# Optimization experiments

Measured on AMD Instinct MI355X. Metric: run time of the kernel, lower is better.

Reference implementation:

```python
import jax, jax.numpy as jnp
import numpy as np

B, Lq, D = 2, 4096, 768
NH, NP, NL = 6, 4, 1
Hs, Ws = 128, 128
Lf = Hs * Ws
DH = D // NH
EPS = 1e-6


def _ln(x, g, b):
    m = jnp.mean(x, -1, keepdims=True)
    v = jnp.mean(jnp.square(x - m), -1, keepdims=True)
    return (x - m) * jax.lax.rsqrt(v + EPS) * g + b


def setup_inputs() -> dict:
    key = jax.random.key(0)
    ks = jax.random.split(key, 20)
    s = 0.02
    rn = lambda k, shape, sc=s: (jax.random.normal(k, shape, jnp.float32) * sc)
    return {
        'query': jax.random.normal(ks[0], (B, Lq, D), jnp.float32),
        'reference_points': jax.random.uniform(ks[1], (B, Lq, NL, 2), jnp.float32),
        'feat': jax.random.normal(ks[2], (B, Lf, D), jnp.float32),
        'feat_other_modalities': jax.random.normal(ks[3], (B, Lq, D), jnp.float32),
        'spatial_shapes': jnp.array([[Hs, Ws]], jnp.int32),
        'level_start_index': jnp.array([0], jnp.int32),
        'qn_g': jnp.ones(D), 'qn_b': jnp.zeros(D),
        'fn_g': jnp.ones(D), 'fn_b': jnp.zeros(D),
        'W_off': rn(ks[4], (D, NH * NL * NP * 2)), 'b_off': jnp.zeros(NH * NL * NP * 2),
        'W_attn': rn(ks[5], (D, NH * NL * NP)), 'b_attn': jnp.zeros(NH * NL * NP),
        'W_val': rn(ks[6], (D, D)), 'b_val': jnp.zeros(D),
        'W_out': rn(ks[7], (D, D)), 'b_out': jnp.zeros(D),
        'gamma': rn(ks[8], (D,), 0.1),
        'qnm_g': jnp.ones(D), 'qnm_b': jnp.zeros(D),
        'fnm_g': jnp.ones(D), 'fnm_b': jnp.zeros(D),
        'ada_w0': rn(ks[9], (D, D // 4)), 'ada_b0': jnp.zeros(D // 4),
        'ada_w1': rn(ks[10], (D, D // 4)), 'ada_b1': jnp.zeros(D // 4),
        'ada_w2': rn(ks[11], (D // 4, D)), 'ada_b2': jnp.zeros(D),
        'gamma_om': rn(ks[12], (D,), 0.1),
    }


def _msdeform_attn(query_n, reference_points, feat_n, Hi, Wi,
                   W_off, b_off, W_attn, b_attn, W_val, b_val, W_out, b_out):
    Bv = query_n.shape[0]
    value = (feat_n @ W_val + b_val).reshape(Bv, Lf, NH, DH)
    value = value.transpose(0, 2, 1, 3)  # (B, NH, Lf, DH)

    off = (query_n @ W_off + b_off).reshape(Bv, Lq, NH, NL, NP, 2)
    aw = (query_n @ W_attn + b_attn).reshape(Bv, Lq, NH, NL * NP)
    aw = jax.nn.softmax(aw, axis=-1).reshape(Bv, Lq, NH, NL, NP)

    normalizer = jnp.array([Wi, Hi], jnp.float32)  # [W, H]
    loc = reference_points[:, :, None, :, None, :] + off / normalizer  # (B,Lq,NH,NL,NP,2)
    loc = loc[:, :, :, 0]  # single level -> (B, Lq, NH, NP, 2)

    # grid_sample align_corners=False, padding zeros
    x = loc[..., 0] * Wi - 0.5
    y = loc[..., 1] * Hi - 0.5
    x0 = jnp.floor(x); y0 = jnp.floor(y)
    wx1 = x - x0; wx0 = 1.0 - wx1
    wy1 = y - y0; wy0 = 1.0 - wy1
    x0i = x0.astype(jnp.int32); y0i = y0.astype(jnp.int32)
    x1i = x0i + 1; y1i = y0i + 1

    def t(a):  # (B,Lq,NH,NP) -> (B,NH,Lq,NP,1)
        return a.transpose(0, 2, 1, 3)[..., None]

    def gather(yy, xx):
        valid = (xx >= 0) & (xx < Wi) & (yy >= 0) & (yy < Hi)
        idx = jnp.clip(yy, 0, Hi - 1) * Wi + jnp.clip(xx, 0, Wi - 1)  # (B,Lq,NH,NP)
        idx = idx.transpose(0, 2, 1, 3).reshape(Bv, NH, Lq * NP)
        g = jnp.take_along_axis(value, idx[..., None], axis=2)  # (B,NH,Lq*NP,DH)
        g = g.reshape(Bv, NH, Lq, NP, DH)
        return g * t(valid.astype(jnp.float32))

    sampled = (gather(y0i, x0i) * t(wy0 * wx0) + gather(y0i, x1i) * t(wy0 * wx1)
               + gather(y1i, x0i) * t(wy1 * wx0) + gather(y1i, x1i) * t(wy1 * wx1))
    awT = aw[:, :, :, 0].transpose(0, 2, 1, 3)[..., None]  # (B,NH,Lq,NP,1)
    out = jnp.sum(sampled * awT, axis=3)  # (B,NH,Lq,DH)
    out = out.transpose(0, 2, 1, 3).reshape(Bv, Lq, D)
    return out @ W_out + b_out


def reference(query, reference_points, feat, feat_other_modalities, spatial_shapes,
              level_start_index, qn_g, qn_b, fn_g, fn_b, W_off, b_off, W_attn, b_attn,
              W_val, b_val, W_out, b_out, gamma, qnm_g, qnm_b, fnm_g, fnm_b,
              ada_w0, ada_b0, ada_w1, ada_b1, ada_w2, ada_b2, gamma_om):
    Hi = int(np.asarray(spatial_shapes)[0, 0]); Wi = int(np.asarray(spatial_shapes)[0, 1])
    query_n = _ln(query, qn_g, qn_b)
    feat_n = _ln(feat, fn_g, fn_b)
    attn = _msdeform_attn(query_n, reference_points, feat_n, Hi, Wi,
                          W_off, b_off, W_attn, b_attn, W_val, b_val, W_out, b_out)
    q = query + gamma * attn
    fom_n = _ln(feat_other_modalities, fnm_g, fnm_b)
    qn2 = _ln(q, qnm_g, qnm_b)
    p = qn2 @ ada_w0 + ada_b0
    xm = fom_n @ ada_w1 + ada_b1
    prompted = (p + xm) @ ada_w2 + ada_b2
    q = q + gamma_om * prompted
    return (q, prompted)
```

## Files before the change

kernel.cpp:

```cpp
#include <hip/hip_runtime.h>
#include <hip/hip_bf16.h>

typedef long long i64;

#define B_   2
#define LQ   4096
#define D_   768
#define NH_  6
#define NP_  4
#define DH_  128
#define LF   16384
#define NQ_ROWS (B_*LQ)
#define NF_ROWS (B_*LF)
#define QSIZE (NQ_ROWS*D_)

typedef __bf16 bf16x8 __attribute__((ext_vector_type(8)));
typedef float  f32x4  __attribute__((ext_vector_type(4)));

__device__ __forceinline__ int probe_bf(const void* probe) {
  return (*(const unsigned*)probe == 0x3F803F80u) ? 1 : 0;
}
__device__ __forceinline__ float load_in(const void* p, i64 i, int bf) {
  if (bf) return __bfloat162float(((const __hip_bfloat16*)p)[i]);
  return ((const float*)p)[i];
}
__device__ __forceinline__ float us2f(unsigned short u) {
  unsigned v = (unsigned)u << 16;
  return __uint_as_float(v);
}
__device__ __forceinline__ unsigned short f2us(float f) {
  __hip_bfloat16 h = __float2bfloat16(f);
  return *(unsigned short*)&h;
}

#define NCVT 17
struct CvtArgs { const void* src[NCVT]; const void* src2[NCVT]; float* dst[NCVT]; int n[NCVT]; const void* probe; };
__global__ void k_cvt(CvtArgs a) {
  int bf = probe_bf(a.probe);
  int ai = blockIdx.y;
  int n = a.n[ai];
  const void* s = a.src[ai];
  const void* s2 = a.src2[ai];
  float* d = a.dst[ai];
  for (int i = blockIdx.x * blockDim.x + threadIdx.x; i < n; i += gridDim.x * blockDim.x) {
    float v = load_in(s, i, bf);
    if (s2) v += load_in(s2, i, bf);
    d[i] = v;
  }
}

#define NTT 7
struct TtArgs {
  const void* src[NTT]; __hip_bfloat16* dst[NTT];
  int K[NTT]; int N[NTT]; int Nt[NTT]; int ds[NTT];
  int tileBase[NTT]; int tilesN[NTT];
  const void* probe;
};
__global__ void k_transpose(TtArgs a) {
  __shared__ float lds[64][65];
  int bf = probe_bf(a.probe);
  int t = blockIdx.x;
  int e = 0;
  #pragma unroll
  for (int i = 1; i < NTT; ++i) if (t >= a.tileBase[i]) e = i;
  int lt = t - a.tileBase[e];
  int tn = lt % a.tilesN[e], tk = lt / a.tilesN[e];
  int K = a.K[e], N = a.N[e], Nt = a.Nt[e], ds = a.ds[e];
  int k0 = tk * 64, n0 = tn * 64;
  int tid = threadIdx.x;
  int cl = tid & 63, rw = tid >> 6;
  const void* s = a.src[e];
  #pragma unroll
  for (int i = 0; i < 16; ++i) {
    int kl = rw * 16 + i;
    int n = n0 + cl;
    float v = (n < N) ? load_in(s, (i64)(k0 + kl) * N + n, bf) : 0.f;
    lds[kl][cl] = v;
  }
  __syncthreads();
  __hip_bfloat16* d = a.dst[e];
  #pragma unroll
  for (int i = 0; i < 16; ++i) {
    int nl = rw * 16 + i;
    int n = n0 + nl;
    if (n < Nt) d[(i64)n * ds + k0 + cl] = __float2bfloat16(lds[cl][nl]);
  }
}


__device__ __forceinline__ void ln_load_bf16(const void* src, i64 so, int sl, uint4* u) {
  const unsigned short* s = (const unsigned short*)src + so;
  #pragma unroll
  for (int j = 0; j < 3; ++j) u[j] = *(const uint4*)(s + (i64)(j * 32 + sl) * 8);
}
__device__ __forceinline__ void ln_load_f32(const void* src, i64 so, int sl, float4* w) {
  const float* s = (const float*)src + so;
  #pragma unroll
  for (int j = 0; j < 3; ++j) {
    w[2*j]   = *(const float4*)(s + (i64)(j * 32 + sl) * 8);
    w[2*j+1] = *(const float4*)(s + (i64)(j * 32 + sl) * 8 + 4);
  }
}
__device__ __forceinline__ void ln_unpack_bf16(const uint4* u, float* v) {
  #pragma unroll
  for (int j = 0; j < 3; ++j) {
    uint4 t = u[j];
    v[j*8+0] = us2f((unsigned short)t.x); v[j*8+1] = us2f((unsigned short)(t.x >> 16));
    v[j*8+2] = us2f((unsigned short)t.y); v[j*8+3] = us2f((unsigned short)(t.y >> 16));
    v[j*8+4] = us2f((unsigned short)t.z); v[j*8+5] = us2f((unsigned short)(t.z >> 16));
    v[j*8+6] = us2f((unsigned short)t.w); v[j*8+7] = us2f((unsigned short)(t.w >> 16));
  }
}
__device__ __forceinline__ void ln_unpack_f32(const float4* w, float* v) {
  #pragma unroll
  for (int j = 0; j < 6; ++j) {
    v[j*4+0] = w[j].x; v[j*4+1] = w[j].y; v[j*4+2] = w[j].z; v[j*4+3] = w[j].w;
  }
}
__device__ __forceinline__ void ln_finish(const float* v, const float* g, const float* b,
                                          unsigned short* dp, int sl) {
  float s1 = 0.f, s2 = 0.f;
  #pragma unroll
  for (int i = 0; i < 24; ++i) { s1 += v[i]; s2 += v[i] * v[i]; }
  #pragma unroll
  for (int o = 16; o > 0; o >>= 1) { s1 += __shfl_xor(s1, o, 64); s2 += __shfl_xor(s2, o, 64); }
  float mean = s1 * (1.f / 768.f);
  float var  = s2 * (1.f / 768.f) - mean * mean;
  float rstd = rsqrtf(var + 1e-6f);
  #pragma unroll
  for (int j = 0; j < 3; ++j) {
    int gi = (j * 32 + sl) * 8;
    float4 g0 = *(const float4*)(g + gi), g1 = *(const float4*)(g + gi + 4);
    float4 b0 = *(const float4*)(b + gi), b1 = *(const float4*)(b + gi + 4);
    uint4 o;
    o.x = (unsigned)f2us((v[j*8+0]-mean)*rstd*g0.x+b0.x) | ((unsigned)f2us((v[j*8+1]-mean)*rstd*g0.y+b0.y) << 16);
    o.y = (unsigned)f2us((v[j*8+2]-mean)*rstd*g0.z+b0.z) | ((unsigned)f2us((v[j*8+3]-mean)*rstd*g0.w+b0.w) << 16);
    o.z = (unsigned)f2us((v[j*8+4]-mean)*rstd*g1.x+b1.x) | ((unsigned)f2us((v[j*8+5]-mean)*rstd*g1.y+b1.y) << 16);
    o.w = (unsigned)f2us((v[j*8+6]-mean)*rstd*g1.z+b1.z) | ((unsigned)f2us((v[j*8+7]-mean)*rstd*g1.w+b1.w) << 16);
    *(uint4*)(dp + gi) = o;
  }
}

struct Ln3Args {
  const void* src0; const void* src1; const void* src2;
  const float *g0, *b0, *g1, *b1, *g2, *b2;
  __hip_bfloat16 *d0, *d1, *d2;
  const void* probe;
};
__device__ __forceinline__ void resolve3(const Ln3Args& a, int row,
    const void*& s, i64& so, const float*& g, const float*& b, unsigned short*& dp) {
  if (row < NF_ROWS) {
    s = a.src0; so = (i64)row * 768; g = a.g0; b = a.b0;
    dp = (unsigned short*)a.d0 + (i64)row * 768;
  } else if (row < NF_ROWS + NQ_ROWS) {
    int r = row - NF_ROWS;
    s = a.src1; so = (i64)r * 768; g = a.g1; b = a.b1;
    dp = (unsigned short*)a.d1 + (i64)r * 768;
  } else {
    int r = row - NF_ROWS - NQ_ROWS;
    s = a.src2; so = (i64)r * 768; g = a.g2; b = a.b2;
    dp = (unsigned short*)a.d2 + (i64)r * 1536 + 768;
  }
}
__global__ void k_ln3(Ln3Args a) {
  int bf = probe_bf(a.probe);
  int hw = blockIdx.x * 8 + (threadIdx.x >> 5);
  int sl = threadIdx.x & 31;
  int row = hw * 2;
  const void* s0; i64 so0; const float *g0, *b0; unsigned short* dp0;
  const void* s1; i64 so1; const float *g1, *b1; unsigned short* dp1;
  resolve3(a, row,     s0, so0, g0, b0, dp0);
  resolve3(a, row + 1, s1, so1, g1, b1, dp1);
  float v[24];
  if (bf) {
    uint4 u0[3], u1[3];
    ln_load_bf16(s0, so0, sl, u0);
    ln_load_bf16(s1, so1, sl, u1);
    ln_unpack_bf16(u0, v);
    ln_finish(v, g0, b0, dp0, sl);
    ln_unpack_bf16(u1, v);
    ln_finish(v, g1, b1, dp1, sl);
  } else {
    float4 w0[6], w1[6];
    ln_load_f32(s0, so0, sl, w0);
    ln_load_f32(s1, so1, sl, w1);
    ln_unpack_f32(w0, v);
    ln_finish(v, g0, b0, dp0, sl);
    ln_unpack_f32(w1, v);
    ln_finish(v, g1, b1, dp1, sl);
  }
}
__global__ void k_ln_q(const float* src, const float* g, const float* b, __hip_bfloat16* dst) {
  int hw = blockIdx.x * 8 + (threadIdx.x >> 5);
  int sl = threadIdx.x & 31;
  int r = hw * 2;
  float4 w0[6], w1[6];
  ln_load_f32(src, (i64)r * 768, sl, w0);
  ln_load_f32(src, (i64)(r + 1) * 768, sl, w1);
  float v[24];
  ln_unpack_f32(w0, v);
  ln_finish(v, g, b, (unsigned short*)dst + (i64)r * 1536, sl);
  ln_unpack_f32(w1, v);
  ln_finish(v, g, b, (unsigned short*)dst + (i64)(r + 1) * 1536, sl);
}

__device__ __forceinline__ void load_lds16(const void* g, void* l) {
  __builtin_amdgcn_global_load_lds((__attribute__((address_space(1))) void*)g,
                                   (__attribute__((address_space(3))) void*)l, 16, 0, 0);
}

template<int EPI>
__global__ void k_mgemm(const __hip_bfloat16* __restrict__ A, const __hip_bfloat16* __restrict__ Wt,
                        const float* __restrict__ bias, void* __restrict__ Cp,
                        int M, int N, int K, int Nx,
                        const void* aux0, const float* __restrict__ aux1, const void* probe) {
  __shared__ __align__(16) __hip_bfloat16 sm[2 * 8192];
  __hip_bfloat16* As = sm;
  __hip_bfloat16* Bs = sm + 8192;
  const int tid  = threadIdx.x;
  const int w    = tid >> 6, lane = tid & 63;
  const int quad = lane >> 4, l15 = lane & 15;
  const int f = blockIdx.x;
  const int xcd = f & 7, s8 = f >> 3;
  const int bn = (s8 % Nx) * 128;
  const int bm = (xcd + (s8 / Nx) * 8) * 128;
  const int wm = (w >> 1) * 64, wn = (w & 1) * 64;
  const int bfv = (EPI == 2 || EPI == 3) ? probe_bf(probe) : 0;

  int rowS[4], colS[4];
  #pragma unroll
  for (int j = 0; j < 4; ++j) {
    int p = j * 256 + tid;
    int r = p >> 3, pc = p & 7;
    rowS[j] = r; colS[j] = (pc ^ (r & 7)) * 8;
  }

  f32x4 acc[4][4];
  #pragma unroll
  for (int i = 0; i < 4; ++i)
    #pragma unroll
    for (int j = 0; j < 4; ++j) acc[i][j] = (f32x4){0.f, 0.f, 0.f, 0.f};

  const __hip_bfloat16* Ab = A  + (i64)bm * K;
  const __hip_bfloat16* Bb = Wt + (i64)bn * K;

  for (int k0 = 0; k0 < K; k0 += 64) {
    #pragma unroll
    for (int j = 0; j < 4; ++j) {
      load_lds16(Ab + (i64)rowS[j] * K + k0 + colS[j], As + (j * 256 + w * 64) * 8);
      load_lds16(Bb + (i64)rowS[j] * K + k0 + colS[j], Bs + (j * 256 + w * 64) * 8);
    }
    __syncthreads();
    bf16x8 af[2][4], bg[2][4];
    #pragma unroll
    for (int s = 0; s < 2; ++s) {
      #pragma unroll
      for (int i = 0; i < 4; ++i) {
        int ra = wm + i * 16 + l15;
        af[s][i] = *(const bf16x8*)(As + (ra * 8 + ((s * 4 + quad) ^ (ra & 7))) * 8);
        int rb = wn + i * 16 + l15;
        bg[s][i] = *(const bf16x8*)(Bs + (rb * 8 + ((s * 4 + quad) ^ (rb & 7))) * 8);
      }
    }
    #pragma unroll
    for (int s = 0; s < 2; ++s)
      #pragma unroll
      for (int i = 0; i < 4; ++i)
        #pragma unroll
        for (int j = 0; j < 4; ++j)
          acc[i][j] = __builtin_amdgcn_mfma_f32_16x16x32_bf16(af[s][i], bg[s][j], acc[i][j], 0, 0, 0);
    __syncthreads();
  }

  #pragma unroll
  for (int j = 0; j < 4; ++j) {
    int col = bn + wn + j * 16 + l15;
    if (col >= N) continue;
    float bv = bias[col];
    #pragma unroll
    for (int i = 0; i < 4; ++i) {
      #pragma unroll
      for (int r = 0; r < 4; ++r) {
        int row = bm + wm + i * 16 + quad * 4 + r;
        float v = acc[i][j][r] + bv;
        i64 idx = (i64)row * N + col;
        if (EPI == 0) {
          ((__hip_bfloat16*)Cp)[idx] = __float2bfloat16(v);
        } else if (EPI == 1) {
          ((float*)Cp)[idx] = v;
        } else if (EPI == 2) {
          ((float*)Cp)[idx] = load_in(aux0, idx, bfv) + aux1[col] * v;
        } else {
          float qv = ((const float*)aux0)[idx] + aux1[col] * v;
          if (bfv) {
            ((__hip_bfloat16*)Cp)[idx]         = __float2bfloat16(qv);
            ((__hip_bfloat16*)Cp)[QSIZE + idx] = __float2bfloat16(v);
          } else {
            ((float*)Cp)[idx]         = qv;
            ((float*)Cp)[QSIZE + idx] = v;
          }
        }
      }
    }
  }
}

__global__ void k_sample(const __hip_bfloat16* __restrict__ val, const float* __restrict__ ref,
                         const float* __restrict__ oa, const int* __restrict__ ss,
                         __hip_bfloat16* __restrict__ out) {
  int gw = blockIdx.x * 4 + (threadIdx.x >> 6);
  if (gw >= NQ_ROWS) return;
  int lane = threadIdx.x & 63;
  int sg = lane >> 4, sl = lane & 15;
  int bq = gw, b = bq >> 12;
  int Hi = ss[0], Wi = ss[1];
  float Wf = (float)Wi, Hf = (float)Hi;
  float rx = ref[(i64)bq*2], ry = ref[(i64)bq*2 + 1];
  const float* orow = oa + (i64)bq * 72;
  const __hip_bfloat16* vb = val + (i64)b * LF * D_;
  int cx = sg & 1, cy = sg >> 1;
  #pragma unroll
  for (int h = 0; h < NH_; ++h) {
    const float* ap = orow + 48 + h*4;
    float a0 = ap[0], a1 = ap[1], a2 = ap[2], a3 = ap[3];
    float mx = fmaxf(fmaxf(a0, a1), fmaxf(a2, a3));
    float e0 = __expf(a0-mx), e1 = __expf(a1-mx), e2 = __expf(a2-mx), e3 = __expf(a3-mx);
    float inv = 1.0f / (e0+e1+e2+e3);
    float wts[4] = {e0*inv, e1*inv, e2*inv, e3*inv};
    const float* op = orow + h*8;
    float acc[8];
    #pragma unroll
    for (int e = 0; e < 8; ++e) acc[e] = 0.f;
    #pragma unroll
    for (int p = 0; p < NP_; ++p) {
      float x = rx*Wf + op[p*2+0] - 0.5f;
      float y = ry*Hf + op[p*2+1] - 0.5f;
      float xf = floorf(x), yf = floorf(y);
      int x0 = (int)xf, y0 = (int)yf;
      float wx1 = x - xf, wy1 = y - yf;
      int xi = x0 + cx, yi = y0 + cy;
      float wgt = wts[p] * (cx ? wx1 : 1.f - wx1) * (cy ? wy1 : 1.f - wy1);
      if (xi >= 0 && xi < Wi && yi >= 0 && yi < Hi) {
        bf16x8 g = *(const bf16x8*)(vb + (i64)(yi*Wi + xi)*D_ + h*DH_ + sl*8);
        #pragma unroll
        for (int e = 0; e < 8; ++e) acc[e] += wgt * (float)g[e];
      }
    }
    #pragma unroll
    for (int e = 0; e < 8; ++e) {
      acc[e] += __shfl_xor(acc[e], 16, 64);
      acc[e] += __shfl_xor(acc[e], 32, 64);
    }
    if (sg == 0) {
      uint4 o;
      o.x = (unsigned)f2us(acc[0]) | ((unsigned)f2us(acc[1]) << 16);
      o.y = (unsigned)f2us(acc[2]) | ((unsigned)f2us(acc[3]) << 16);
      o.z = (unsigned)f2us(acc[4]) | ((unsigned)f2us(acc[5]) << 16);
      o.w = (unsigned)f2us(acc[6]) | ((unsigned)f2us(acc[7]) << 16);
      *(uint4*)(out + (i64)bq*D_ + h*DH_ + sl*8) = o;
    }
  }
}

extern "C" void kernel_launch(void* const* d_in, const int* in_sizes, int n_in,
                              void* d_out, int out_size, void* d_ws, size_t ws_size,
                              hipStream_t stream) {
  char* base = (char*)d_ws;
  size_t o = 0;
  auto alloc = [&](size_t bytes) { size_t r = o; o += (bytes + 63) & ~(size_t)63; return r; };
  auto F = [&](size_t off) { return (float*)(base + off); };
  auto H = [&](size_t off) { return (__hip_bfloat16*)(base + off); };
  const void* probe = d_in[6];

  size_t REF   = alloc(NQ_ROWS*2*4);
  size_t QN_G  = alloc(768*4); size_t QN_B = alloc(768*4);
  size_t FN_G  = alloc(768*4); size_t FN_B = alloc(768*4);
  size_t BOA   = alloc(128*4);
  size_t BVAL  = alloc(768*4); size_t BOUT = alloc(768*4);
  size_t GAMMA = alloc(768*4);
  size_t QNM_G = alloc(768*4); size_t QNM_B = alloc(768*4);
  size_t FNM_G = alloc(768*4); size_t FNM_B = alloc(768*4);
  size_t AB01  = alloc(192*4);
  size_t AB2   = alloc(768*4); size_t GOM  = alloc(768*4);
  size_t WT_VAL = alloc((size_t)768*768*2);
  size_t WT_OUT = alloc((size_t)768*768*2);
  size_t WT_OA  = alloc((size_t)128*768*2);
  size_t WT_A01 = alloc((size_t)256*1536*2);
  size_t WT_A2  = alloc((size_t)768*192*2);
  size_t FEATN  = alloc((size_t)NF_ROWS*768*2);
  size_t VALUE  = alloc((size_t)NF_ROWS*768*2);
  size_t QN     = alloc((size_t)NQ_ROWS*768*2);
  size_t QNF    = alloc((size_t)NQ_ROWS*1536*2);
  size_t ATTNP  = alloc((size_t)NQ_ROWS*768*2);
  size_t PXM    = alloc((size_t)NQ_ROWS*192*2);
  size_t OA     = alloc((size_t)NQ_ROWS*72*4);
  size_t QBUF   = alloc((size_t)QSIZE*4);

  {
    CvtArgs ca;
    const int   idx[NCVT]  = {1,6,7,8,9,11,13,15,17,18,19,20,21,22,24,28,29};
    const size_t dof[NCVT] = {REF,QN_G,QN_B,FN_G,FN_B,BOA,BOA+48*4,BVAL,BOUT,GAMMA,
                              QNM_G,QNM_B,FNM_G,FNM_B,AB01,AB2,GOM};
    for (int i = 0; i < NCVT; ++i) {
      ca.src[i] = d_in[idx[i]]; ca.src2[i] = nullptr;
      ca.dst[i] = F(dof[i]); ca.n[i] = in_sizes[idx[i]];
    }
    ca.src2[14] = d_in[26];
    ca.probe = probe;
    k_cvt<<<dim3(8, NCVT), 256, 0, stream>>>(ca);
  }
  {
    TtArgs ta;
    const int   src[NTT]  = {14, 16, 10, 12, 23, 25, 27};
    const size_t dst[NTT] = {WT_VAL, WT_OUT, WT_OA, WT_OA + (size_t)48*768*2,
                             WT_A01, WT_A01 + (size_t)768*2, WT_A2};
    const int Kk[NTT] = {768, 768, 768, 768, 768,  768, 192};
    const int Nn[NTT] = {768, 768,  48,  24, 192,  192, 768};
    const int Nt[NTT] = {768, 768,  48,  80, 256,  256, 768};
    const int Ds[NTT] = {768, 768, 768, 768, 1536, 1536, 192};
    int tb = 0;
    for (int i = 0; i < NTT; ++i) {
      ta.src[i] = d_in[src[i]]; ta.dst[i] = H(dst[i]);
      ta.K[i] = Kk[i]; ta.N[i] = Nn[i]; ta.Nt[i] = Nt[i]; ta.ds[i] = Ds[i];
      ta.tilesN[i] = (Nt[i] + 63) / 64;
      ta.tileBase[i] = tb;
      tb += ta.tilesN[i] * (Kk[i] / 64);
    }
    ta.probe = probe;
    k_transpose<<<tb, 256, 0, stream>>>(ta);
  }

  {
    Ln3Args la;
    la.src0 = d_in[2]; la.g0 = F(FN_G);  la.b0 = F(FN_B);  la.d0 = H(FEATN);
    la.src1 = d_in[0]; la.g1 = F(QN_G);  la.b1 = F(QN_B);  la.d1 = H(QN);
    la.src2 = d_in[3]; la.g2 = F(FNM_G); la.b2 = F(FNM_B); la.d2 = H(QNF);
    la.probe = probe;
    k_ln3<<<(NF_ROWS + 2*NQ_ROWS) / 16, 256, 0, stream>>>(la);
  }

  k_mgemm<0><<<256*6, 256, 0, stream>>>(H(FEATN), H(WT_VAL), F(BVAL), H(VALUE),
                                        NF_ROWS, 768, 768, 6, nullptr, nullptr, probe);
  k_mgemm<1><<<64*1, 256, 0, stream>>>(H(QN), H(WT_OA), F(BOA), F(OA),
                                       NQ_ROWS, 72, 768, 1, nullptr, nullptr, probe);
  k_sample<<<NQ_ROWS/4, 256, 0, stream>>>(H(VALUE), F(REF), F(OA), (const int*)d_in[4], H(ATTNP));
  k_mgemm<2><<<64*6, 256, 0, stream>>>(H(ATTNP), H(WT_OUT), F(BOUT), F(QBUF),
                                       NQ_ROWS, 768, 768, 6, d_in[0], F(GAMMA), probe);
  k_ln_q<<<NQ_ROWS/16, 256, 0, stream>>>(F(QBUF), F(QNM_G), F(QNM_B), H(QNF));
  k_mgemm<0><<<64*2, 256, 0, stream>>>(H(QNF), H(WT_A01), F(AB01), H(PXM),
                                       NQ_ROWS, 192, 1536, 2, nullptr, nullptr, probe);
  k_mgemm<3><<<64*6, 256, 0, stream>>>(H(PXM), H(WT_A2), F(AB2), d_out,
                                       NQ_ROWS, 768, 192, 6, F(QBUF), F(GOM), probe);
}
```

Measured before the change: 480.7 us.

## Fold layernorm of feat and query into GEMM epilogues via row stats

Instead of writing normalized bf16 feat/query, the pre-pass computes per-row rstd and -mean*rstd, and folds gamma into the transposed weights. The GEMM epilogue reconstructs LN(x)@W as rstd*acc + rc*colsum(gW) + colsum(bW) + bias. A small colsum kernel computes these vectors. With bf16 inputs the raw input is fed straight to the GEMM, skipping the normalized write. With fp32 inputs it still writes an unnormalized bf16 copy. The pre-pass is also made grid-stride with software prefetch. The trade-off is some precision loss, since unnormalized values are rounded to bf16 before the matmul.

```diff
diff --git a/kernel.cpp b/kernel.cpp
--- a/kernel.cpp
+++ b/kernel.cpp
@@ -13,6 +13,7 @@
 #define NQ_ROWS (B_*LQ)
 #define NF_ROWS (B_*LF)
 #define QSIZE (NQ_ROWS*D_)
+#define R_TOT (NF_ROWS + 2*NQ_ROWS)
 
 typedef __bf16 bf16x8 __attribute__((ext_vector_type(8)));
 typedef float  f32x4  __attribute__((ext_vector_type(4)));
@@ -52,6 +53,7 @@
 #define NTT 7
 struct TtArgs {
   const void* src[NTT]; __hip_bfloat16* dst[NTT];
+  const void* scale[NTT];
   int K[NTT]; int N[NTT]; int Nt[NTT]; int ds[NTT];
   int tileBase[NTT]; int tilesN[NTT];
   const void* probe;
@@ -70,11 +72,13 @@
   int tid = threadIdx.x;
   int cl = tid & 63, rw = tid >> 6;
   const void* s = a.src[e];
+  const void* sc = a.scale[e];
   #pragma unroll
   for (int i = 0; i < 16; ++i) {
     int kl = rw * 16 + i;
     int n = n0 + cl;
     float v = (n < N) ? load_in(s, (i64)(k0 + kl) * N + n, bf) : 0.f;
+    if (sc) v *= load_in(sc, k0 + kl, bf);
     lds[kl][cl] = v;
   }
   __syncthreads();
@@ -87,6 +91,30 @@
   }
 }
 
+#define NCS 3
+struct CsArgs {
+  const void* w[NCS]; const void* g[NCS]; const void* b[NCS];
+  float* c[NCS]; float* d[NCS];
+  int K[NCS]; int N[NCS]; int blkBase[NCS];
+  const void* probe;
+};
+__global__ void k_colsum(CsArgs a) {
+  int bf = probe_bf(a.probe);
+  int e = 0;
+  #pragma unroll
+  for (int i = 1; i < NCS; ++i) if ((int)blockIdx.x >= a.blkBase[i]) e = i;
+  int j = (blockIdx.x - a.blkBase[e]) * 256 + threadIdx.x;
+  int K = a.K[e], N = a.N[e];
+  if (j >= N) return;
+  const void* w = a.w[e]; const void* g = a.g[e]; const void* b = a.b[e];
+  float cs = 0.f, ds = 0.f;
+  for (int k = 0; k < K; ++k) {
+    float wv = load_in(w, (i64)k * N + j, bf);
+    cs += load_in(g, k, bf) * wv;
+    ds += load_in(b, k, bf) * wv;
+  }
+  a.c[e][j] = cs; a.d[e][j] = ds;
+}
 
 __device__ __forceinline__ void ln_load_bf16(const void* src, i64 so, int sl, uint4* u) {
   const unsigned short* s = (const unsigned short*)src + so;
@@ -117,8 +145,7 @@
     v[j*4+0] = w[j].x; v[j*4+1] = w[j].y; v[j*4+2] = w[j].z; v[j*4+3] = w[j].w;
   }
 }
-__device__ __forceinline__ void ln_finish(const float* v, const float* g, const float* b,
-                                          unsigned short* dp, int sl) {
+__device__ __forceinline__ void pre_stats(const float* v, float& rstd, float& rc) {
   float s1 = 0.f, s2 = 0.f;
   #pragma unroll
   for (int i = 0; i < 24; ++i) { s1 += v[i]; s2 += v[i] * v[i]; }
@@ -126,7 +153,14 @@
   for (int o = 16; o > 0; o >>= 1) { s1 += __shfl_xor(s1, o, 64); s2 += __shfl_xor(s2, o, 64); }
   float mean = s1 * (1.f / 768.f);
   float var  = s2 * (1.f / 768.f) - mean * mean;
-  float rstd = rsqrtf(var + 1e-6f);
+  rstd = rsqrtf(var + 1e-6f);
+  rc = -rstd * mean;
+}
+__device__ __forceinline__ void ln_finish(const float* v, const float* g, const float* b,
+                                          unsigned short* dp, int sl) {
+  float rstd, rc;
+  pre_stats(v, rstd, rc);
+  float mean = -rc / rstd;
   #pragma unroll
   for (int j = 0; j < 3; ++j) {
     int gi = (j * 32 + sl) * 8;
@@ -140,56 +174,83 @@
     *(uint4*)(dp + gi) = o;
   }
 }
-
-struct Ln3Args {
-  const void* src0; const void* src1; const void* src2;
-  const float *g0, *b0, *g1, *b1, *g2, *b2;
-  __hip_bfloat16 *d0, *d1, *d2;
+__device__ __forceinline__ void pack_store(const float* v, unsigned short* dp, int sl) {
+  #pragma unroll
+  for (int j = 0; j < 3; ++j) {
+    int gi = (j * 32 + sl) * 8;
+    uint4 o;
+    o.x = (unsigned)f2us(v[j*8+0]) | ((unsigned)f2us(v[j*8+1]) << 16);
+    o.y = (unsigned)f2us(v[j*8+2]) | ((unsigned)f2us(v[j*8+3]) << 16);
+    o.z = (unsigned)f2us(v[j*8+4]) | ((unsigned)f2us(v[j*8+5]) << 16);
+    o.w = (unsigned)f2us(v[j*8+6]) | ((unsigned)f2us(v[j*8+7]) << 16);
+    *(uint4*)(dp + gi) = o;
+  }
+}
+
+struct PreArgs {
+  const void* feat; const void* query; const void* fom;
+  const float *fg, *fb;
+  float* fstat; float* qstat;
+  __hip_bfloat16* feat_bf; __hip_bfloat16* q_bf;
+  __hip_bfloat16* qnf;
   const void* probe;
 };
-__device__ __forceinline__ void resolve3(const Ln3Args& a, int row,
-    const void*& s, i64& so, const float*& g, const float*& b, unsigned short*& dp) {
-  if (row < NF_ROWS) {
-    s = a.src0; so = (i64)row * 768; g = a.g0; b = a.b0;
-    dp = (unsigned short*)a.d0 + (i64)row * 768;
-  } else if (row < NF_ROWS + NQ_ROWS) {
-    int r = row - NF_ROWS;
-    s = a.src1; so = (i64)r * 768; g = a.g1; b = a.b1;
-    dp = (unsigned short*)a.d1 + (i64)r * 768;
+__device__ __forceinline__ void pre_src(const PreArgs& a, int row,
+    const void*& s, i64& so, int& kind, int& lr) {
+  if (row < NF_ROWS)                { s = a.feat;  lr = row;                       so = (i64)lr * 768; kind = 0; }
+  else if (row < NF_ROWS + NQ_ROWS) { s = a.query; lr = row - NF_ROWS;            so = (i64)lr * 768; kind = 1; }
+  else                              { s = a.fom;   lr = row - NF_ROWS - NQ_ROWS;  so = (i64)lr * 768; kind = 2; }
+}
+__global__ void k_pre(PreArgs a) {
+  int bf = probe_bf(a.probe);
+  int sl = threadIdx.x & 31;
+  int stride = gridDim.x * 8;
+  int r = blockIdx.x * 8 + (threadIdx.x >> 5);
+  if (bf) {
+    uint4 u[3]; const void* s; i64 so; int kind = 0, lr = 0;
+    if (r < R_TOT) { pre_src(a, r, s, so, kind, lr); ln_load_bf16(s, so, sl, u); }
+    while (r < R_TOT) {
+      int rn = r + stride;
+      uint4 un[3]; const void* sn; i64 son; int kn = 0, lrn = 0;
+      if (rn < R_TOT) { pre_src(a, rn, sn, son, kn, lrn); ln_load_bf16(sn, son, sl, un); }
+      float v[24];
+      ln_unpack_bf16(u, v);
+      if (kind == 2) {
+        ln_finish(v, a.fg, a.fb, (unsigned short*)a.qnf + (i64)lr * 1536 + 768, sl);
+      } else {
+        float rstd, rc; pre_stats(v, rstd, rc);
+        float* st = (kind == 0) ? a.fstat : a.qstat;
+        if (sl == 0) { st[2*lr] = rstd; st[2*lr+1] = rc; }
+      }
+      r = rn; kind = kn; lr = lrn;
+      u[0] = un[0]; u[1] = un[1]; u[2] = un[2];
+    }
   } else {
-    int r = row - NF_ROWS - NQ_ROWS;
-    s = a.src2; so = (i64)r * 768; g = a.g2; b = a.b2;
-    dp = (unsigned short*)a.d2 + (i64)r * 1536 + 768;
-  }
-}
-__global__ void k_ln3(Ln3Args a) {
-  int bf = probe_bf(a.probe);
-  int hw = blockIdx.x * 8 + (threadIdx.x >> 5);
-  int sl = threadIdx.x & 31;
-  int row = hw * 2;
-  const void* s0; i64 so0; const float *g0, *b0; unsigned short* dp0;
-  const void* s1; i64 so1; const float *g1, *b1; unsigned short* dp1;
-  resolve3(a, row,     s0, so0, g0, b0, dp0);
-  resolve3(a, row + 1, s1, so1, g1, b1, dp1);
-  float v[24];
-  if (bf) {
-    uint4 u0[3], u1[3];
-    ln_load_bf16(s0, so0, sl, u0);
-    ln_load_bf16(s1, so1, sl, u1);
-    ln_unpack_bf16(u0, v);
-    ln_finish(v, g0, b0, dp0, sl);
-    ln_unpack_bf16(u1, v);
-    ln_finish(v, g1, b1, dp1, sl);
-  } else {
-    float4 w0[6], w1[6];
-    ln_load_f32(s0, so0, sl, w0);
-    ln_load_f32(s1, so1, sl, w1);
-    ln_unpack_f32(w0, v);
-    ln_finish(v, g0, b0, dp0, sl);
-    ln_unpack_f32(w1, v);
-    ln_finish(v, g1, b1, dp1, sl);
-  }
-}
+    float4 w[6]; const void* s; i64 so; int kind = 0, lr = 0;
+    if (r < R_TOT) { pre_src(a, r, s, so, kind, lr); ln_load_f32(s, so, sl, w); }
+    while (r < R_TOT) {
+      int rn = r + stride;
+      float4 wn[6]; const void* sn; i64 son; int kn = 0, lrn = 0;
+      if (rn < R_TOT) { pre_src(a, rn, sn, son, kn, lrn); ln_load_f32(sn, son, sl, wn); }
+      float v[24];
+      ln_unpack_f32(w, v);
+      if (kind == 2) {
+        ln_finish(v, a.fg, a.fb, (unsigned short*)a.qnf + (i64)lr * 1536 + 768, sl);
+      } else {
+        float rstd, rc; pre_stats(v, rstd, rc);
+        float* st = (kind == 0) ? a.fstat : a.qstat;
+        if (sl == 0) { st[2*lr] = rstd; st[2*lr+1] = rc; }
+        unsigned short* dp = (kind == 0) ? (unsigned short*)a.feat_bf + (i64)lr * 768
+                                         : (unsigned short*)a.q_bf + (i64)lr * 768;
+        pack_store(v, dp, sl);
+      }
+      r = rn; kind = kn; lr = lrn;
+      #pragma unroll
+      for (int i = 0; i < 6; ++i) w[i] = wn[i];
+    }
+  }
+}
+
 __global__ void k_ln_q(const float* src, const float* g, const float* b, __hip_bfloat16* dst) {
   int hw = blockIdx.x * 8 + (threadIdx.x >> 5);
   int sl = threadIdx.x & 31;
@@ -213,7 +274,8 @@
 __global__ void k_mgemm(const __hip_bfloat16* __restrict__ A, const __hip_bfloat16* __restrict__ Wt,
                         const float* __restrict__ bias, void* __restrict__ Cp,
                         int M, int N, int K, int Nx,
-                        const void* aux0, const float* __restrict__ aux1, const void* probe) {
+                        const void* aux0, const float* __restrict__ aux1,
+                        const float* __restrict__ aux2, const void* Araw, const void* probe) {
   __shared__ __align__(16) __hip_bfloat16 sm[2 * 8192];
   __hip_bfloat16* As = sm;
   __hip_bfloat16* Bs = sm + 8192;
@@ -225,7 +287,9 @@
   const int bn = (s8 % Nx) * 128;
   const int bm = (xcd + (s8 / Nx) * 8) * 128;
   const int wm = (w >> 1) * 64, wn = (w & 1) * 64;
-  const int bfv = (EPI == 2 || EPI == 3) ? probe_bf(probe) : 0;
+  const int bfv = (EPI >= 2) ? probe_bf(probe) : 0;
+  const __hip_bfloat16* Ause = A;
+  if (EPI == 4 || EPI == 5) Ause = bfv ? (const __hip_bfloat16*)Araw : A;
 
   int rowS[4], colS[4];
   #pragma unroll
@@ -241,8 +305,8 @@
     #pragma unroll
     for (int j = 0; j < 4; ++j) acc[i][j] = (f32x4){0.f, 0.f, 0.f, 0.f};
 
-  const __hip_bfloat16* Ab = A  + (i64)bm * K;
-  const __hip_bfloat16* Bb = Wt + (i64)bn * K;
+  const __hip_bfloat16* Ab = Ause + (i64)bm * K;
+  const __hip_bfloat16* Bb = Wt   + (i64)bn * K;
 
   for (int k0 = 0; k0 < K; k0 += 64) {
     #pragma unroll
@@ -282,15 +346,21 @@
       #pragma unroll
       for (int r = 0; r < 4; ++r) {
         int row = bm + wm + i * 16 + quad * 4 + r;
-        float v = acc[i][j][r] + bv;
         i64 idx = (i64)row * N + col;
-        if (EPI == 0) {
+        float v;
+        if (EPI == 4 || EPI == 5) {
+          const float* rst = (const float*)aux0;
+          v = rst[2*row] * acc[i][j][r] + rst[2*row+1] * aux1[col] + aux2[col] + bv;
+        } else {
+          v = acc[i][j][r] + bv;
+        }
+        if (EPI == 0 || EPI == 4) {
           ((__hip_bfloat16*)Cp)[idx] = __float2bfloat16(v);
-        } else if (EPI == 1) {
+        } else if (EPI == 1 || EPI == 5) {
           ((float*)Cp)[idx] = v;
         } else if (EPI == 2) {
           ((float*)Cp)[idx] = load_in(aux0, idx, bfv) + aux1[col] * v;
-        } else {
+        } else if (EPI == 3) {
           float qv = ((const float*)aux0)[idx] + aux1[col] * v;
           if (bfv) {
             ((__hip_bfloat16*)Cp)[idx]         = __float2bfloat16(qv);
@@ -382,14 +452,18 @@
   size_t FNM_G = alloc(768*4); size_t FNM_B = alloc(768*4);
   size_t AB01  = alloc(192*4);
   size_t AB2   = alloc(768*4); size_t GOM  = alloc(768*4);
+  size_t CV    = alloc(768*4); size_t DV   = alloc(768*4);
+  size_t CO    = alloc(128*4); size_t DO_  = alloc(128*4);
+  size_t FSTAT = alloc((size_t)NF_ROWS*2*4);
+  size_t QSTAT = alloc((size_t)NQ_ROWS*2*4);
   size_t WT_VAL = alloc((size_t)768*768*2);
   size_t WT_OUT = alloc((size_t)768*768*2);
   size_t WT_OA  = alloc((size_t)128*768*2);
   size_t WT_A01 = alloc((size_t)256*1536*2);
   size_t WT_A2  = alloc((size_t)768*192*2);
-  size_t FEATN  = alloc((size_t)NF_ROWS*768*2);
+  size_t FEAT_BF = alloc((size_t)NF_ROWS*768*2);
+  size_t Q_BF    = alloc((size_t)NQ_ROWS*768*2);
   size_t VALUE  = alloc((size_t)NF_ROWS*768*2);
-  size_t QN     = alloc((size_t)NQ_ROWS*768*2);
   size_t QNF    = alloc((size_t)NQ_ROWS*1536*2);
   size_t ATTNP  = alloc((size_t)NQ_ROWS*768*2);
   size_t PXM    = alloc((size_t)NQ_ROWS*192*2);
@@ -418,9 +492,10 @@
     const int Nn[NTT] = {768, 768,  48,  24, 192,  192, 768};
     const int Nt[NTT] = {768, 768,  48,  80, 256,  256, 768};
     const int Ds[NTT] = {768, 768, 768, 768, 1536, 1536, 192};
+    const void* sc[NTT] = {d_in[8], nullptr, d_in[6], d_in[6], nullptr, nullptr, nullptr};
     int tb = 0;
     for (int i = 0; i < NTT; ++i) {
-      ta.src[i] = d_in[src[i]]; ta.dst[i] = H(dst[i]);
+      ta.src[i] = d_in[src[i]]; ta.dst[i] = H(dst[i]); ta.scale[i] = sc[i];
       ta.K[i] = Kk[i]; ta.N[i] = Nn[i]; ta.Nt[i] = Nt[i]; ta.ds[i] = Ds[i];
       ta.tilesN[i] = (Nt[i] + 63) / 64;
       ta.tileBase[i] = tb;
@@ -429,26 +504,51 @@
     ta.probe = probe;
     k_transpose<<<tb, 256, 0, stream>>>(ta);
   }
-
   {
-    Ln3Args la;
-    la.src0 = d_in[2]; la.g0 = F(FN_G);  la.b0 = F(FN_B);  la.d0 = H(FEATN);
-    la.src1 = d_in[0]; la.g1 = F(QN_G);  la.b1 = F(QN_B);  la.d1 = H(QN);
-    la.src2 = d_in[3]; la.g2 = F(FNM_G); la.b2 = F(FNM_B); la.d2 = H(QNF);
-    la.probe = probe;
-    k_ln3<<<(NF_ROWS + 2*NQ_ROWS) / 16, 256, 0, stream>>>(la);
-  }
-
-  k_mgemm<0><<<256*6, 256, 0, stream>>>(H(FEATN), H(WT_VAL), F(BVAL), H(VALUE),
-                                        NF_ROWS, 768, 768, 6, nullptr, nullptr, probe);
-  k_mgemm<1><<<64*1, 256, 0, stream>>>(H(QN), H(WT_OA), F(BOA), F(OA),
-                                       NQ_ROWS, 72, 768, 1, nullptr, nullptr, probe);
+    CsArgs cs;
+    const void* ws[NCS] = {d_in[14], d_in[10], d_in[12]};
+    const void* gs[NCS] = {d_in[8],  d_in[6],  d_in[6]};
+    const void* bs[NCS] = {d_in[9],  d_in[7],  d_in[7]};
+    float* cp[NCS] = {F(CV), F(CO), F(CO) + 48};
+    float* dp[NCS] = {F(DV), F(DO_), F(DO_) + 48};
+    const int Kk[NCS] = {768, 768, 768};
+    const int Nn[NCS] = {768, 48, 24};
+    const int bb[NCS] = {0, 3, 4};
+    for (int i = 0; i < NCS; ++i) {
+      cs.w[i] = ws[i]; cs.g[i] = gs[i]; cs.b[i] = bs[i];
+      cs.c[i] = cp[i]; cs.d[i] = dp[i];
+      cs.K[i] = Kk[i]; cs.N[i] = Nn[i]; cs.blkBase[i] = bb[i];
+    }
+    cs.probe = probe;
+    k_colsum<<<5, 256, 0, stream>>>(cs);
+  }
+
+  {
+    PreArgs pa;
+    pa.feat = d_in[2]; pa.query = d_in[0]; pa.fom = d_in[3];
+    pa.fg = F(FNM_G); pa.fb = F(FNM_B);
+    pa.fstat = F(FSTAT); pa.qstat = F(QSTAT);
+    pa.feat_bf = H(FEAT_BF); pa.q_bf = H(Q_BF);
+    pa.qnf = H(QNF);
+    pa.probe = probe;
+    k_pre<<<1024, 256, 0, stream>>>(pa);
+  }
+
+  k_mgemm<4><<<256*6, 256, 0, stream>>>(H(FEAT_BF), H(WT_VAL), F(BVAL), H(VALUE),
+                                        NF_ROWS, 768, 768, 6,
+                                        F(FSTAT), F(CV), F(DV), d_in[2], probe);
+  k_mgemm<5><<<64*1, 256, 0, stream>>>(H(Q_BF), H(WT_OA), F(BOA), F(OA),
+                                       NQ_ROWS, 72, 768, 1,
+                                       F(QSTAT), F(CO), F(DO_), d_in[0], probe);
   k_sample<<<NQ_ROWS/4, 256, 0, stream>>>(H(VALUE), F(REF), F(OA), (const int*)d_in[4], H(ATTNP));
   k_mgemm<2><<<64*6, 256, 0, stream>>>(H(ATTNP), H(WT_OUT), F(BOUT), F(QBUF),
-                                       NQ_ROWS, 768, 768, 6, d_in[0], F(GAMMA), probe);
+                                       NQ_ROWS, 768, 768, 6,
+                                       d_in[0], F(GAMMA), nullptr, nullptr, probe);
   k_ln_q<<<NQ_ROWS/16, 256, 0, stream>>>(F(QBUF), F(QNM_G), F(QNM_B), H(QNF));
   k_mgemm<0><<<64*2, 256, 0, stream>>>(H(QNF), H(WT_A01), F(AB01), H(PXM),
-                                       NQ_ROWS, 192, 1536, 2, nullptr, nullptr, probe);
+                                       NQ_ROWS, 192, 1536, 2,
+                                       nullptr, nullptr, nullptr, nullptr, probe);
   k_mgemm<3><<<64*6, 256, 0, stream>>>(H(PXM), H(WT_A2), F(AB2), d_out,
-                                       NQ_ROWS, 768, 192, 6, F(QBUF), F(GOM), probe);
-}
+                                       NQ_ROWS, 768, 192, 6,
+                                       F(QBUF), F(GOM), nullptr, nullptr, probe);
+}
```

Measured after the change: 737.3 us. 53.4% more time.
